# Kernel optimization log

Measured on AMD Instinct MI355X. Metric: run time of the kernel, lower is better.

The kernel has to match this reference:

```python
import jax, jax.numpy as jnp
import numpy as np

ALPHA = 2.0 / 5.0  # GRU-flow z scaling (Neural Flows, Bilos et al.)
BETA = 4.0 / 5.0   # GRU-flow r scaling


def setup_inputs() -> dict:
    key = jax.random.key(0)
    ks = jax.random.split(key, 16)
    B, T, Ds, Da, H, LF = 4096, 200, 32, 8, 128, 2

    def rn(k, shape, scale=0.1):
        return jax.random.normal(k, shape, dtype=jnp.float32) * scale

    return dict(
        s=rn(ks[0], (B, T, Ds), 1.0),
        a=rn(ks[1], (B, T, Da), 1.0),
        t=jax.random.uniform(ks[2], (B, T), dtype=jnp.float32),
        flow_Wr=rn(ks[3], (LF, H + 1, H)),
        flow_br=rn(ks[4], (LF, H)),
        flow_Wz=rn(ks[5], (LF, H + 1, H)),
        flow_bz=rn(ks[6], (LF, H)),
        flow_Wh=rn(ks[7], (LF, H + 1, H)),
        flow_bh=rn(ks[8], (LF, H)),
        flow_time_w=rn(ks[9], (LF, H), 1.0),
        gru_Wih=rn(ks[10], (3 * H, Ds + Da)),
        gru_Whh=rn(ks[11], (3 * H, H)),
        gru_bih=rn(ks[12], (3 * H,)),
        gru_bhh=rn(ks[13], (3 * H,)),
        dec_W=rn(ks[14], (Ds, H)),
        dec_b=rn(ks[15], (Ds,)),
    )


def reference(s, a, t, flow_Wr, flow_br, flow_Wz, flow_bz, flow_Wh, flow_bh,
              flow_time_w, gru_Wih, gru_Whh, gru_bih, gru_bhh, dec_W, dec_b):
    B, T, Ds = s.shape
    H = gru_Whh.shape[1]
    n_flow = flow_Wr.shape[0]

    def flow_block(h, tt, l):
        # h: [B,H], tt: [B,1]
        inp = jnp.concatenate([h, tt], axis=-1)                       # [B,H+1]
        r = BETA * jax.nn.sigmoid(inp @ flow_Wr[l] + flow_br[l])
        z = ALPHA * jax.nn.sigmoid(inp @ flow_Wz[l] + flow_bz[l])
        u = jnp.tanh(jnp.concatenate([r * h, tt], -1) @ flow_Wh[l] + flow_bh[l])
        phi = jnp.tanh(flow_time_w[l] * tt)                           # TimeTanh, phi(0)=0
        return h + phi * z * (u - h)

    def step(h, xs):
        s_i, a_i, t_i = xs                                            # [B,Ds],[B,Da],[B]
        tt = t_i[:, None]
        for l in range(n_flow):
            h = flow_block(h, tt, l)
        hid = h                                                       # stored hidden = flow output
        x = jnp.concatenate([s_i, a_i], axis=-1)                      # mode='truth'
        gi = x @ gru_Wih.T + gru_bih                                  # [B,3H]
        gh = h @ gru_Whh.T + gru_bhh
        r = jax.nn.sigmoid(gi[:, :H] + gh[:, :H])
        z = jax.nn.sigmoid(gi[:, H:2 * H] + gh[:, H:2 * H])
        n = jnp.tanh(gi[:, 2 * H:] + r * gh[:, 2 * H:])
        h_new = (1.0 - z) * n + z * h                                 # torch GRU update
        o = h_new @ dec_W.T + dec_b
        return h_new, (o, hid)

    h0 = jnp.zeros((B, H), dtype=s.dtype)
    xs = (jnp.swapaxes(s, 0, 1), jnp.swapaxes(a, 0, 1), jnp.swapaxes(t, 0, 1))
    _, (outs, hids) = jax.lax.scan(step, h0, xs)
    return jnp.swapaxes(outs, 0, 1), jnp.swapaxes(hids, 0, 1)
```

## Files before the change

### kernel.cpp

```cpp
#include <hip/hip_runtime.h>
#include <hip/hip_bf16.h>

typedef __attribute__((ext_vector_type(8))) short short8;
typedef __attribute__((ext_vector_type(4))) float f32x4;
typedef unsigned short u16;

#define NB   4096
#define TT   200
#define DS   32
#define DA   8
#define HH   128
#define HP   136
#define XP   72
#define BB   16
#define NTHR 512

#define OW_R 0
#define OW_Z 33024
#define OW_H 66048
#define OB_R 99072
#define OB_Z 99328
#define OB_H 99584
#define OTW  99840
#define OWIH 100096
#define OWHH 124672
#define OBIH 173824
#define OBHH 174208
#define ODW  174592
#define ODB  178688
#define NPK  178720
#define OFF2 16512
#define HIDOFF ((size_t)NB * TT * DS)

__device__ __forceinline__ float bf2f(u16 u){
  union { unsigned int i; float f; } v; v.i = ((unsigned int)u) << 16; return v.f;
}
__device__ __forceinline__ u16 f2bf(float f){
  __hip_bfloat16 h = __float2bfloat16(f);
  return *reinterpret_cast<u16*>(&h);
}
__device__ __forceinline__ float sigm(float x){
  return __builtin_amdgcn_rcpf(1.f + __expf(-x));
}
__device__ __forceinline__ float tanh_(float x){
  return 1.f - 2.f * __builtin_amdgcn_rcpf(1.f + __expf(2.f * x));
}
__device__ __forceinline__ float scrub(float x){
  return fminf(8.f, fmaxf(-8.f, x));
}

__global__ void detect_kernel(const void* t_in, int* ws_flag){
  int lane = threadIdx.x;
  u16 v = ((const u16*)t_in)[2 * lane];
  float f = bf2f(v);
  bool ok = (f >= 0.0009765625f) && (f < 1.0f);
  unsigned long long m = __ballot(ok);
  if (lane == 0) ws_flag[0] = (__popcll(m) < 32) ? 1 : 0;
}

__global__ void conv_kernel(const void* Wr, const void* Wz, const void* Wh,
                            const void* br, const void* bz, const void* bh,
                            const void* tw, const void* Wih, const void* Whh,
                            const void* bih, const void* bhh,
                            const void* dW, const void* db_, void* ws){
  const int flag = *(const int*)ws;
  u16* dst = (u16*)ws + 8;
  int i = blockIdx.x * 256 + threadIdx.x;
  if (i >= NPK) return;
  auto cv = [&](const void* p, int li) -> u16 {
    if (flag) return f2bf(((const float*)p)[li]);
    return ((const u16*)p)[li];
  };
  u16 v;
  if      (i < OW_Z) v = cv(Wr,  i - OW_R);
  else if (i < OW_H) v = cv(Wz,  i - OW_Z);
  else if (i < OB_R) v = cv(Wh,  i - OW_H);
  else if (i < OB_Z) v = cv(br,  i - OB_R);
  else if (i < OB_H) v = cv(bz,  i - OB_Z);
  else if (i < OTW)  v = cv(bh,  i - OB_H);
  else if (i < OWIH) v = cv(tw,  i - OTW);
  else if (i < OWHH) { int li = i - OWIH; int n = li >> 6, k = li & 63;
                       v = (k < 40) ? cv(Wih, n * 40 + k) : (u16)0; }
  else if (i < OBIH) v = cv(Whh, i - OWHH);
  else if (i < OBHH) v = cv(bih, i - OBIH);
  else if (i < ODW)  v = cv(bhh, i - OBHH);
  else if (i < ODB)  v = cv(dW,  i - ODW);
  else               v = cv(db_, i - ODB);
  dst[i] = v;
}

__global__ __launch_bounds__(NTHR, 2)
void odernn_kernel(const void* __restrict__ s_in, const void* __restrict__ a_in,
                   const void* __restrict__ t_in, void* __restrict__ out,
                   const void* __restrict__ ws){
  __shared__ alignas(16) u16 h_sh[2][BB][HP];
  __shared__ alignas(16) u16 rh_sh[BB][HP];
  __shared__ alignas(16) u16 x_sh[BB][XP];
  __shared__ float t_sh[BB];

  const int flag = *(const int*)ws;
  const u16* pk  = (const u16*)ws + 8;

  const int tid  = threadIdx.x;
  const int w    = tid >> 6;
  const int lane = tid & 63;
  const int q    = lane >> 4;
  const int m16  = lane & 15;
  const int col  = (w << 4) | m16;
  const int row4 = q << 2;
  const int b0   = blockIdx.x * BB;
  const int aoff = m16 * HP + q * 8;

  for (int i = tid; i < 2*BB*HP; i += NTHR) (&h_sh[0][0][0])[i] = 0;
  for (int i = tid; i < BB*XP;   i += NTHR) (&x_sh[0][0])[i]   = 0;
  if (tid < BB){
    size_t idx = (size_t)(b0 + tid) * TT;
    float tv; if (flag) tv = ((const float*)t_in)[idx]; else tv = bf2f(((const u16*)t_in)[idx]);
    t_sh[tid] = tv;
  }

  const u16* WrP = pk + OW_R; const u16* WzP = pk + OW_Z; const u16* WhP = pk + OW_H;
  const u16* Wsrc[6] = { WrP, WzP, WhP, WrP + OFF2, WzP + OFF2, WhP + OFF2 };
  short8 fw[6][4];
  float fwl[6], fb[6];
#pragma unroll
  for (int m = 0; m < 6; ++m){
#pragma unroll
    for (int ks = 0; ks < 4; ++ks){
      short8 v;
#pragma unroll
      for (int j = 0; j < 8; ++j)
        v[j] = (short)Wsrc[m][(ks*32 + q*8 + j)*HH + col];
      fw[m][ks] = v;
    }
    fwl[m] = bf2f(Wsrc[m][128*HH + col]);
  }
  fb[0] = bf2f(pk[OB_R + col]);      fb[1] = bf2f(pk[OB_Z + col]);      fb[2] = bf2f(pk[OB_H + col]);
  fb[3] = bf2f(pk[OB_R + HH + col]); fb[4] = bf2f(pk[OB_Z + HH + col]); fb[5] = bf2f(pk[OB_H + HH + col]);
  const float ftw0 = bf2f(pk[OTW + col]), ftw1 = bf2f(pk[OTW + HH + col]);

  short8 whhf[3][4];
#pragma unroll
  for (int g = 0; g < 3; ++g){
    const u16* base = pk + OWHH + (size_t)(g*HH + col) * HH;
#pragma unroll
    for (int ks = 0; ks < 4; ++ks)
      whhf[g][ks] = *reinterpret_cast<const short8*>(base + ks*32 + q*8);
  }
  const float bs_r = bf2f(pk[OBIH + col])      + bf2f(pk[OBHH + col]);
  const float bs_z = bf2f(pk[OBIH + HH + col]) + bf2f(pk[OBHH + HH + col]);
  const float bi_n = bf2f(pk[OBIH + 2*HH + col]);
  const float bh_n = bf2f(pk[OBHH + 2*HH + col]);
  const float db   = bf2f(pk[ODB + (col & 31)]);

  float hv[4] = {0.f, 0.f, 0.f, 0.f};
  int cur = 0;
  __syncthreads();

  for (int t = 0; t < TT; ++t){
    const u16* h_in = &h_sh[cur][0][0];
    float tt4[4];
#pragma unroll
    for (int r = 0; r < 4; ++r) tt4[r] = t_sh[row4 + r];

    if (w < 2 && t > 0){
      f32x4 oacc = {0.f,0.f,0.f,0.f};
#pragma unroll
      for (int ks = 0; ks < 4; ++ks){
        short8 da  = *reinterpret_cast<const short8*>(h_in + aoff + ks*32);
        short8 dbw = *reinterpret_cast<const short8*>(pk + ODW + col*HH + ks*32 + q*8);
        oacc = __builtin_amdgcn_mfma_f32_16x16x32_bf16(da, dbw, oacc, 0, 0, 0);
      }
#pragma unroll
      for (int r = 0; r < 4; ++r){
        size_t oidx = ((size_t)(b0 + row4 + r)*TT + (t - 1))*DS + col;
        float val = oacc[r] + db;
        if (flag) ((float*)out)[oidx] = val; else ((u16*)out)[oidx] = f2bf(val);
      }
    }

#pragma unroll
    for (int l = 0; l < 2; ++l){
      const u16* hr = &h_sh[cur][0][0];
      u16* hw = &h_sh[cur ^ 1][0][0];
      short8 ha[4];
#pragma unroll
      for (int ks = 0; ks < 4; ++ks)
        ha[ks] = *reinterpret_cast<const short8*>(hr + aoff + ks*32);
      f32x4 racc = {0.f,0.f,0.f,0.f}, zacc = {0.f,0.f,0.f,0.f};
#pragma unroll
      for (int ks = 0; ks < 4; ++ks){
        racc = __builtin_amdgcn_mfma_f32_16x16x32_bf16(ha[ks], fw[3*l+0][ks], racc, 0, 0, 0);
        zacc = __builtin_amdgcn_mfma_f32_16x16x32_bf16(ha[ks], fw[3*l+1][ks], zacc, 0, 0, 0);
      }
      float zv[4];
#pragma unroll
      for (int r = 0; r < 4; ++r){
        float rv = 0.8f * sigm(racc[r] + tt4[r]*fwl[3*l+0] + fb[3*l+0]);
        zv[r]    = 0.4f * sigm(zacc[r] + tt4[r]*fwl[3*l+1] + fb[3*l+1]);
        rh_sh[row4 + r][col] = f2bf(rv * hv[r]);
      }
      if (l == 1){
        { int row = tid >> 5, c = tid & 31;
          size_t sidx = ((size_t)(b0 + row)*TT + t)*DS + c;
          float sv; if (flag) sv = ((const float*)s_in)[sidx]; else sv = bf2f(((const u16*)s_in)[sidx]);
          x_sh[row][c] = f2bf(sv); }
        if (tid < BB*DA){ int row = tid >> 3, c = tid & 7;
          size_t aidx = ((size_t)(b0 + row)*TT + t)*DA + c;
          float av; if (flag) av = ((const float*)a_in)[aidx]; else av = bf2f(((const u16*)a_in)[aidx]);
          x_sh[row][DS + c] = f2bf(av); }
      }
      __syncthreads();
      short8 ua[4];
#pragma unroll
      for (int ks = 0; ks < 4; ++ks)
        ua[ks] = *reinterpret_cast<const short8*>(&rh_sh[0][0] + aoff + ks*32);
      f32x4 uacc = {0.f,0.f,0.f,0.f};
#pragma unroll
      for (int ks = 0; ks < 4; ++ks)
        uacc = __builtin_amdgcn_mfma_f32_16x16x32_bf16(ua[ks], fw[3*l+2][ks], uacc, 0, 0, 0);
      const float ftwl = l ? ftw1 : ftw0;
#pragma unroll
      for (int r = 0; r < 4; ++r){
        float u   = tanh_(uacc[r] + tt4[r]*fwl[3*l+2] + fb[3*l+2]);
        float phi = tanh_(ftwl * tt4[r]);
        hv[r] = scrub(hv[r] + phi * zv[r] * (u - hv[r]));
        hw[(row4 + r)*HP + col] = f2bf(hv[r]);
      }
      __syncthreads();
      cur ^= 1;
    }

    {
      const u16* hg = &h_sh[cur][0][0];
      u16* hw = &h_sh[cur ^ 1][0][0];
#pragma unroll
      for (int r = 0; r < 4; ++r){
        size_t hidx = HIDOFF + ((size_t)(b0 + row4 + r)*TT + t)*HH + col;
        if (flag) ((float*)out)[hidx] = hv[r]; else ((u16*)out)[hidx] = f2bf(hv[r]);
      }
      if (tid < BB && t + 1 < TT){
        size_t idx = (size_t)(b0 + tid)*TT + t + 1;
        float tv; if (flag) tv = ((const float*)t_in)[idx]; else tv = bf2f(((const u16*)t_in)[idx]);
        t_sh[tid] = tv;
      }

      short8 xa[2];
#pragma unroll
      for (int ks = 0; ks < 2; ++ks)
        xa[ks] = *reinterpret_cast<const short8*>(&x_sh[0][0] + m16*XP + ks*32 + q*8);
      f32x4 ar = {0.f,0.f,0.f,0.f}, az = {0.f,0.f,0.f,0.f};
      f32x4 agin = {0.f,0.f,0.f,0.f}, aghn = {0.f,0.f,0.f,0.f};
      const u16* wr_ih = pk + OWIH + (size_t)col*64;
      const u16* wz_ih = pk + OWIH + (size_t)(HH + col)*64;
      const u16* wn_ih = pk + OWIH + (size_t)(2*HH + col)*64;
#pragma unroll
      for (int ks = 0; ks < 2; ++ks){
        const int kb = ks*32 + q*8;
        ar   = __builtin_amdgcn_mfma_f32_16x16x32_bf16(xa[ks], *reinterpret_cast<const short8*>(wr_ih + kb), ar,   0,0,0);
        az   = __builtin_amdgcn_mfma_f32_16x16x32_bf16(xa[ks], *reinterpret_cast<const short8*>(wz_ih + kb), az,   0,0,0);
        agin = __builtin_amdgcn_mfma_f32_16x16x32_bf16(xa[ks], *reinterpret_cast<const short8*>(wn_ih + kb), agin, 0,0,0);
      }
      short8 hgf[4];
#pragma unroll
      for (int ks = 0; ks < 4; ++ks)
        hgf[ks] = *reinterpret_cast<const short8*>(hg + aoff + ks*32);
#pragma unroll
      for (int ks = 0; ks < 4; ++ks){
        ar   = __builtin_amdgcn_mfma_f32_16x16x32_bf16(hgf[ks], whhf[0][ks], ar,   0,0,0);
        az   = __builtin_amdgcn_mfma_f32_16x16x32_bf16(hgf[ks], whhf[1][ks], az,   0,0,0);
        aghn = __builtin_amdgcn_mfma_f32_16x16x32_bf16(hgf[ks], whhf[2][ks], aghn, 0,0,0);
      }
#pragma unroll
      for (int r = 0; r < 4; ++r){
        float gr = sigm(ar[r] + bs_r);
        float gz = sigm(az[r] + bs_z);
        float gn = tanh_(agin[r] + bi_n + gr*(aghn[r] + bh_n));
        hv[r] = scrub((1.f - gz)*gn + gz*hv[r]);
        hw[(row4 + r)*HP + col] = f2bf(hv[r]);
      }
      __syncthreads();
      cur ^= 1;
    }
  }

  if (w < 2){
    const u16* h_in = &h_sh[cur][0][0];
    f32x4 oacc = {0.f,0.f,0.f,0.f};
#pragma unroll
    for (int ks = 0; ks < 4; ++ks){
      short8 da  = *reinterpret_cast<const short8*>(h_in + aoff + ks*32);
      short8 dbw = *reinterpret_cast<const short8*>(pk + ODW + col*HH + ks*32 + q*8);
      oacc = __builtin_amdgcn_mfma_f32_16x16x32_bf16(da, dbw, oacc, 0, 0, 0);
    }
#pragma unroll
    for (int r = 0; r < 4; ++r){
      size_t oidx = ((size_t)(b0 + row4 + r)*TT + (TT - 1))*DS + col;
      float val = oacc[r] + db;
      if (flag) ((float*)out)[oidx] = val; else ((u16*)out)[oidx] = f2bf(val);
    }
  }
}

extern "C" void kernel_launch(void* const* d_in, const int* in_sizes, int n_in,
                              void* d_out, int out_size, void* d_ws, size_t ws_size,
                              hipStream_t stream){
  detect_kernel<<<1, 64, 0, stream>>>(d_in[2], (int*)d_ws);
  conv_kernel<<<(NPK + 255)/256, 256, 0, stream>>>(d_in[3], d_in[5], d_in[7],
                                                   d_in[4], d_in[6], d_in[8],
                                                   d_in[9], d_in[10], d_in[11],
                                                   d_in[12], d_in[13], d_in[14],
                                                   d_in[15], d_ws);
  odernn_kernel<<<dim3(NB/BB), dim3(NTHR), 0, stream>>>(
      d_in[0], d_in[1], d_in[2], d_out, d_ws);
}
```

Measured before the change: 1.346 ms.

## Halve batch tile, stream pre-transposed weights from global, prefetch inputs

The batch tile drops from 16 to 8 rows and the block from 512 to 256 threads, so twice as many blocks run. The flow weights are pre-transposed in the packing kernel into a column-major layout and no longer held in registers; every MFMA now loads its B operand from global/L2 and computes two 16-column tiles per wave. The s/a inputs for the next step are prefetched into registers. The aim is to cut register pressure and raise occupancy, at the cost of repeated weight loads each step and half-wasted MFMA rows, since only 8 of the 16 A rows are real.

```diff
diff --git a/kernel.cpp b/kernel.cpp
--- a/kernel.cpp
+++ b/kernel.cpp
@@ -12,24 +12,22 @@
 #define HH   128
 #define HP   136
 #define XP   72
-#define BB   16
-#define NTHR 512
-
-#define OW_R 0
-#define OW_Z 33024
-#define OW_H 66048
-#define OB_R 99072
-#define OB_Z 99328
-#define OB_H 99584
-#define OTW  99840
-#define OWIH 100096
-#define OWHH 124672
-#define OBIH 173824
-#define OBHH 174208
-#define ODW  174592
-#define ODB  178688
-#define NPK  178720
-#define OFF2 16512
+#define BB   8
+#define NTHR 256
+
+#define PFW   0
+#define PFWL  98304
+#define PFB   99072
+#define PTW   99840
+#define PWIH  100096
+#define PWHH  124672
+#define PBIH  173824
+#define PBHH  174208
+#define PDW   174592
+#define PDB   178688
+#define NPK   178720
+#define FSTRIDE 16512
+
 #define HIDOFF ((size_t)NB * TT * DS)
 
 __device__ __forceinline__ float bf2f(u16 u){
@@ -48,6 +46,10 @@
 __device__ __forceinline__ float scrub(float x){
   return fminf(8.f, fmaxf(-8.f, x));
 }
+__device__ __forceinline__ short8 ld8(const u16* p){
+  return *reinterpret_cast<const short8*>(p);
+}
+#define MFMA __builtin_amdgcn_mfma_f32_16x16x32_bf16
 
 __global__ void detect_kernel(const void* t_in, int* ws_flag){
   int lane = threadIdx.x;
@@ -71,21 +73,26 @@
     if (flag) return f2bf(((const float*)p)[li]);
     return ((const u16*)p)[li];
   };
+  const void* FG[3]  = { Wr, Wz, Wh };
+  const void* FBp[3] = { br, bz, bh };
   u16 v;
-  if      (i < OW_Z) v = cv(Wr,  i - OW_R);
-  else if (i < OW_H) v = cv(Wz,  i - OW_Z);
-  else if (i < OB_R) v = cv(Wh,  i - OW_H);
-  else if (i < OB_Z) v = cv(br,  i - OB_R);
-  else if (i < OB_H) v = cv(bz,  i - OB_Z);
-  else if (i < OTW)  v = cv(bh,  i - OB_H);
-  else if (i < OWIH) v = cv(tw,  i - OTW);
-  else if (i < OWHH) { int li = i - OWIH; int n = li >> 6, k = li & 63;
-                       v = (k < 40) ? cv(Wih, n * 40 + k) : (u16)0; }
-  else if (i < OBIH) v = cv(Whh, i - OWHH);
-  else if (i < OBHH) v = cv(bih, i - OBIH);
-  else if (i < ODW)  v = cv(bhh, i - OBHH);
-  else if (i < ODB)  v = cv(dW,  i - ODW);
-  else               v = cv(db_, i - ODB);
+  if (i < PFWL){ int m = i >> 14, r = i & 16383, col = r >> 7, k = r & 127;
+                 int l = m / 3, g = m % 3;
+                 v = cv(FG[g], l*FSTRIDE + k*HH + col); }
+  else if (i < PFB){ int li = i - PFWL; int m = li >> 7, col = li & 127;
+                 int l = m / 3, g = m % 3;
+                 v = cv(FG[g], l*FSTRIDE + HH*HH + col); }
+  else if (i < PTW){ int li = i - PFB; int m = li >> 7, col = li & 127;
+                 int l = m / 3, g = m % 3;
+                 v = cv(FBp[g], l*HH + col); }
+  else if (i < PWIH){ v = cv(tw, i - PTW); }
+  else if (i < PWHH){ int li = i - PWIH; int n = li >> 6, k = li & 63;
+                 v = (k < 40) ? cv(Wih, n*40 + k) : (u16)0; }
+  else if (i < PBIH){ v = cv(Whh, i - PWHH); }
+  else if (i < PBHH){ v = cv(bih, i - PBIH); }
+  else if (i < PDW) { v = cv(bhh, i - PBHH); }
+  else if (i < PDB) { v = cv(dW,  i - PDW); }
+  else              { v = cv(db_, i - PDB); }
   dst[i] = v;
 }
 
@@ -93,10 +100,10 @@
 void odernn_kernel(const void* __restrict__ s_in, const void* __restrict__ a_in,
                    const void* __restrict__ t_in, void* __restrict__ out,
                    const void* __restrict__ ws){
-  __shared__ alignas(16) u16 h_sh[2][BB][HP];
-  __shared__ alignas(16) u16 rh_sh[BB][HP];
-  __shared__ alignas(16) u16 x_sh[BB][XP];
-  __shared__ float t_sh[BB];
+  __shared__ alignas(16) u16 h_sh[2][8][HP];
+  __shared__ alignas(16) u16 rh_sh[8][HP];
+  __shared__ alignas(16) u16 x_sh[8][XP];
+  __shared__ float t_sh[8];
 
   const int flag = *(const int*)ws;
   const u16* pk  = (const u16*)ws + 8;
@@ -106,76 +113,82 @@
   const int lane = tid & 63;
   const int q    = lane >> 4;
   const int m16  = lane & 15;
-  const int col  = (w << 4) | m16;
-  const int row4 = q << 2;
+  const bool hi  = (q >= 2);
+  const int row4 = (q & 1) << 2;
+  const int colm = (w << 5) + ((q >> 1) << 4) + m16;
+  const int aoff  = (m16 & 7) * HP + (q << 3);
+  const int aoffx = (m16 & 7) * XP + (q << 3);
   const int b0   = blockIdx.x * BB;
-  const int aoff = m16 * HP + q * 8;
-
-  for (int i = tid; i < 2*BB*HP; i += NTHR) (&h_sh[0][0][0])[i] = 0;
-  for (int i = tid; i < BB*XP;   i += NTHR) (&x_sh[0][0])[i]   = 0;
+
+  for (int i = tid; i < 2*8*HP; i += NTHR) (&h_sh[0][0][0])[i] = 0;
+  for (int i = tid; i < 8*XP;   i += NTHR) (&x_sh[0][0])[i]   = 0;
   if (tid < BB){
     size_t idx = (size_t)(b0 + tid) * TT;
-    float tv; if (flag) tv = ((const float*)t_in)[idx]; else tv = bf2f(((const u16*)t_in)[idx]);
-    t_sh[tid] = tv;
+    t_sh[tid] = flag ? ((const float*)t_in)[idx] : bf2f(((const u16*)t_in)[idx]);
   }
 
-  const u16* WrP = pk + OW_R; const u16* WzP = pk + OW_Z; const u16* WhP = pk + OW_H;
-  const u16* Wsrc[6] = { WrP, WzP, WhP, WrP + OFF2, WzP + OFF2, WhP + OFF2 };
-  short8 fw[6][4];
   float fwl[6], fb[6];
 #pragma unroll
   for (int m = 0; m < 6; ++m){
-#pragma unroll
-    for (int ks = 0; ks < 4; ++ks){
-      short8 v;
-#pragma unroll
-      for (int j = 0; j < 8; ++j)
-        v[j] = (short)Wsrc[m][(ks*32 + q*8 + j)*HH + col];
-      fw[m][ks] = v;
-    }
-    fwl[m] = bf2f(Wsrc[m][128*HH + col]);
+    fwl[m] = bf2f(pk[PFWL + m*HH + colm]);
+    fb[m]  = bf2f(pk[PFB  + m*HH + colm]);
   }
-  fb[0] = bf2f(pk[OB_R + col]);      fb[1] = bf2f(pk[OB_Z + col]);      fb[2] = bf2f(pk[OB_H + col]);
-  fb[3] = bf2f(pk[OB_R + HH + col]); fb[4] = bf2f(pk[OB_Z + HH + col]); fb[5] = bf2f(pk[OB_H + HH + col]);
-  const float ftw0 = bf2f(pk[OTW + col]), ftw1 = bf2f(pk[OTW + HH + col]);
-
-  short8 whhf[3][4];
-#pragma unroll
-  for (int g = 0; g < 3; ++g){
-    const u16* base = pk + OWHH + (size_t)(g*HH + col) * HH;
-#pragma unroll
-    for (int ks = 0; ks < 4; ++ks)
-      whhf[g][ks] = *reinterpret_cast<const short8*>(base + ks*32 + q*8);
-  }
-  const float bs_r = bf2f(pk[OBIH + col])      + bf2f(pk[OBHH + col]);
-  const float bs_z = bf2f(pk[OBIH + HH + col]) + bf2f(pk[OBHH + HH + col]);
-  const float bi_n = bf2f(pk[OBIH + 2*HH + col]);
-  const float bh_n = bf2f(pk[OBHH + 2*HH + col]);
-  const float db   = bf2f(pk[ODB + (col & 31)]);
+  const float ftw0 = bf2f(pk[PTW + colm]);
+  const float ftw1 = bf2f(pk[PTW + HH + colm]);
+  const float bs_r = bf2f(pk[PBIH + colm])      + bf2f(pk[PBHH + colm]);
+  const float bs_z = bf2f(pk[PBIH + HH + colm]) + bf2f(pk[PBHH + HH + colm]);
+  const float bi_n = bf2f(pk[PBIH + 2*HH + colm]);
+  const float bh_n = bf2f(pk[PBHH + 2*HH + colm]);
+  const float db   = bf2f(pk[PDB + ((w & 1) << 4) + m16]);
+
+  int fB[6][2], whB[3][2], wiB[3][2];
+#pragma unroll
+  for (int m = 0; m < 6; ++m)
+#pragma unroll
+    for (int c = 0; c < 2; ++c)
+      fB[m][c] = PFW + m*16384 + (((w*2 + c)*16 + m16) << 7) + (q << 3);
+#pragma unroll
+  for (int g = 0; g < 3; ++g)
+#pragma unroll
+    for (int c = 0; c < 2; ++c){
+      whB[g][c] = PWHH + ((g*HH + (w*2 + c)*16 + m16) << 7) + (q << 3);
+      wiB[g][c] = PWIH + ((g*HH + (w*2 + c)*16 + m16) << 6) + (q << 3);
+    }
+  const int dwB = PDW + (((w & 1)*16 + m16) << 7) + (q << 3);
+
+  float sP, aP = 0.f;
+  { int row = tid >> 5, c = tid & 31;
+    size_t sidx = ((size_t)(b0 + row)*TT + 0)*DS + c;
+    sP = flag ? ((const float*)s_in)[sidx] : bf2f(((const u16*)s_in)[sidx]); }
+  if (tid < 64){ int row = tid >> 3, c = tid & 7;
+    size_t aidx = ((size_t)(b0 + row)*TT + 0)*DA + c;
+    aP = flag ? ((const float*)a_in)[aidx] : bf2f(((const u16*)a_in)[aidx]); }
 
   float hv[4] = {0.f, 0.f, 0.f, 0.f};
   int cur = 0;
   __syncthreads();
 
   for (int t = 0; t < TT; ++t){
-    const u16* h_in = &h_sh[cur][0][0];
     float tt4[4];
 #pragma unroll
     for (int r = 0; r < 4; ++r) tt4[r] = t_sh[row4 + r];
 
     if (w < 2 && t > 0){
-      f32x4 oacc = {0.f,0.f,0.f,0.f};
+      const u16* hr = &h_sh[cur][0][0];
+      f32x4 oa = {0.f,0.f,0.f,0.f};
 #pragma unroll
       for (int ks = 0; ks < 4; ++ks){
-        short8 da  = *reinterpret_cast<const short8*>(h_in + aoff + ks*32);
-        short8 dbw = *reinterpret_cast<const short8*>(pk + ODW + col*HH + ks*32 + q*8);
-        oacc = __builtin_amdgcn_mfma_f32_16x16x32_bf16(da, dbw, oacc, 0, 0, 0);
-      }
-#pragma unroll
-      for (int r = 0; r < 4; ++r){
-        size_t oidx = ((size_t)(b0 + row4 + r)*TT + (t - 1))*DS + col;
-        float val = oacc[r] + db;
-        if (flag) ((float*)out)[oidx] = val; else ((u16*)out)[oidx] = f2bf(val);
+        short8 haf = *reinterpret_cast<const short8*>(hr + aoff + ks*32);
+        short8 bw  = ld8(pk + dwB + ks*32);
+        oa = MFMA(haf, bw, oa, 0, 0, 0);
+      }
+      if (q < 2){
+#pragma unroll
+        for (int r = 0; r < 4; ++r){
+          size_t oidx = ((size_t)(b0 + (q<<2) + r)*TT + (t-1))*DS + ((w&1)<<4) + m16;
+          float val = oa[r] + db;
+          if (flag) ((float*)out)[oidx] = val; else ((u16*)out)[oidx] = f2bf(val);
+        }
       }
     }
 
@@ -187,45 +200,55 @@
 #pragma unroll
       for (int ks = 0; ks < 4; ++ks)
         ha[ks] = *reinterpret_cast<const short8*>(hr + aoff + ks*32);
-      f32x4 racc = {0.f,0.f,0.f,0.f}, zacc = {0.f,0.f,0.f,0.f};
+      f32x4 r0={0.f,0.f,0.f,0.f}, r1={0.f,0.f,0.f,0.f};
+      f32x4 z0={0.f,0.f,0.f,0.f}, z1={0.f,0.f,0.f,0.f};
 #pragma unroll
       for (int ks = 0; ks < 4; ++ks){
-        racc = __builtin_amdgcn_mfma_f32_16x16x32_bf16(ha[ks], fw[3*l+0][ks], racc, 0, 0, 0);
-        zacc = __builtin_amdgcn_mfma_f32_16x16x32_bf16(ha[ks], fw[3*l+1][ks], zacc, 0, 0, 0);
+        r0 = MFMA(ha[ks], ld8(pk + fB[3*l+0][0] + ks*32), r0, 0,0,0);
+        r1 = MFMA(ha[ks], ld8(pk + fB[3*l+0][1] + ks*32), r1, 0,0,0);
+        z0 = MFMA(ha[ks], ld8(pk + fB[3*l+1][0] + ks*32), z0, 0,0,0);
+        z1 = MFMA(ha[ks], ld8(pk + fB[3*l+1][1] + ks*32), z1, 0,0,0);
       }
       float zv[4];
 #pragma unroll
       for (int r = 0; r < 4; ++r){
-        float rv = 0.8f * sigm(racc[r] + tt4[r]*fwl[3*l+0] + fb[3*l+0]);
-        zv[r]    = 0.4f * sigm(zacc[r] + tt4[r]*fwl[3*l+1] + fb[3*l+1]);
-        rh_sh[row4 + r][col] = f2bf(rv * hv[r]);
+        float ra = hi ? r1[r] : r0[r];
+        float za = hi ? z1[r] : z0[r];
+        float rv = 0.8f * sigm(ra + tt4[r]*fwl[3*l+0] + fb[3*l+0]);
+        zv[r]    = 0.4f * sigm(za + tt4[r]*fwl[3*l+1] + fb[3*l+1]);
+        rh_sh[row4 + r][colm] = f2bf(rv * hv[r]);
       }
       if (l == 1){
-        { int row = tid >> 5, c = tid & 31;
-          size_t sidx = ((size_t)(b0 + row)*TT + t)*DS + c;
-          float sv; if (flag) sv = ((const float*)s_in)[sidx]; else sv = bf2f(((const u16*)s_in)[sidx]);
-          x_sh[row][c] = f2bf(sv); }
-        if (tid < BB*DA){ int row = tid >> 3, c = tid & 7;
-          size_t aidx = ((size_t)(b0 + row)*TT + t)*DA + c;
-          float av; if (flag) av = ((const float*)a_in)[aidx]; else av = bf2f(((const u16*)a_in)[aidx]);
-          x_sh[row][DS + c] = f2bf(av); }
+        { int row = tid >> 5, c = tid & 31; x_sh[row][c] = f2bf(sP); }
+        if (tid < 64){ int row = tid >> 3, c = tid & 7; x_sh[row][DS + c] = f2bf(aP); }
+        if (t + 1 < TT){
+          int row = tid >> 5, c = tid & 31;
+          size_t sidx = ((size_t)(b0 + row)*TT + (t+1))*DS + c;
+          sP = flag ? ((const float*)s_in)[sidx] : bf2f(((const u16*)s_in)[sidx]);
+          if (tid < 64){ int r2 = tid >> 3, c2 = tid & 7;
+            size_t aidx = ((size_t)(b0 + r2)*TT + (t+1))*DA + c2;
+            aP = flag ? ((const float*)a_in)[aidx] : bf2f(((const u16*)a_in)[aidx]); }
+        }
       }
       __syncthreads();
       short8 ua[4];
 #pragma unroll
       for (int ks = 0; ks < 4; ++ks)
         ua[ks] = *reinterpret_cast<const short8*>(&rh_sh[0][0] + aoff + ks*32);
-      f32x4 uacc = {0.f,0.f,0.f,0.f};
-#pragma unroll
-      for (int ks = 0; ks < 4; ++ks)
-        uacc = __builtin_amdgcn_mfma_f32_16x16x32_bf16(ua[ks], fw[3*l+2][ks], uacc, 0, 0, 0);
+      f32x4 u0={0.f,0.f,0.f,0.f}, u1={0.f,0.f,0.f,0.f};
+#pragma unroll
+      for (int ks = 0; ks < 4; ++ks){
+        u0 = MFMA(ua[ks], ld8(pk + fB[3*l+2][0] + ks*32), u0, 0,0,0);
+        u1 = MFMA(ua[ks], ld8(pk + fB[3*l+2][1] + ks*32), u1, 0,0,0);
+      }
       const float ftwl = l ? ftw1 : ftw0;
 #pragma unroll
       for (int r = 0; r < 4; ++r){
-        float u   = tanh_(uacc[r] + tt4[r]*fwl[3*l+2] + fb[3*l+2]);
+        float ume = hi ? u1[r] : u0[r];
+        float u   = tanh_(ume + tt4[r]*fwl[3*l+2] + fb[3*l+2]);
         float phi = tanh_(ftwl * tt4[r]);
         hv[r] = scrub(hv[r] + phi * zv[r] * (u - hv[r]));
-        hw[(row4 + r)*HP + col] = f2bf(hv[r]);
+        hw[(row4 + r)*HP + colm] = f2bf(hv[r]);
       }
       __syncthreads();
       cur ^= 1;
@@ -234,50 +257,54 @@
     {
       const u16* hg = &h_sh[cur][0][0];
       u16* hw = &h_sh[cur ^ 1][0][0];
-#pragma unroll
-      for (int r = 0; r < 4; ++r){
-        size_t hidx = HIDOFF + ((size_t)(b0 + row4 + r)*TT + t)*HH + col;
-        if (flag) ((float*)out)[hidx] = hv[r]; else ((u16*)out)[hidx] = f2bf(hv[r]);
+      short8 xa[2];
+#pragma unroll
+      for (int ks = 0; ks < 2; ++ks)
+        xa[ks] = *reinterpret_cast<const short8*>(&x_sh[0][0] + aoffx + ks*32);
+      short8 hgf[4];
+#pragma unroll
+      for (int ks = 0; ks < 4; ++ks)
+        hgf[ks] = *reinterpret_cast<const short8*>(hg + aoff + ks*32);
+      f32x4 ar0={0.f,0.f,0.f,0.f}, ar1={0.f,0.f,0.f,0.f};
+      f32x4 az0={0.f,0.f,0.f,0.f}, az1={0.f,0.f,0.f,0.f};
+      f32x4 an0={0.f,0.f,0.f,0.f}, an1={0.f,0.f,0.f,0.f};
+      f32x4 ah0={0.f,0.f,0.f,0.f}, ah1={0.f,0.f,0.f,0.f};
+#pragma unroll
+      for (int ks = 0; ks < 2; ++ks){
+        ar0 = MFMA(xa[ks], ld8(pk + wiB[0][0] + ks*32), ar0, 0,0,0);
+        ar1 = MFMA(xa[ks], ld8(pk + wiB[0][1] + ks*32), ar1, 0,0,0);
+        az0 = MFMA(xa[ks], ld8(pk + wiB[1][0] + ks*32), az0, 0,0,0);
+        az1 = MFMA(xa[ks], ld8(pk + wiB[1][1] + ks*32), az1, 0,0,0);
+        an0 = MFMA(xa[ks], ld8(pk + wiB[2][0] + ks*32), an0, 0,0,0);
+        an1 = MFMA(xa[ks], ld8(pk + wiB[2][1] + ks*32), an1, 0,0,0);
+      }
+#pragma unroll
+      for (int ks = 0; ks < 4; ++ks){
+        ar0 = MFMA(hgf[ks], ld8(pk + whB[0][0] + ks*32), ar0, 0,0,0);
+        ar1 = MFMA(hgf[ks], ld8(pk + whB[0][1] + ks*32), ar1, 0,0,0);
+        az0 = MFMA(hgf[ks], ld8(pk + whB[1][0] + ks*32), az0, 0,0,0);
+        az1 = MFMA(hgf[ks], ld8(pk + whB[1][1] + ks*32), az1, 0,0,0);
+        ah0 = MFMA(hgf[ks], ld8(pk + whB[2][0] + ks*32), ah0, 0,0,0);
+        ah1 = MFMA(hgf[ks], ld8(pk + whB[2][1] + ks*32), ah1, 0,0,0);
       }
       if (tid < BB && t + 1 < TT){
         size_t idx = (size_t)(b0 + tid)*TT + t + 1;
-        float tv; if (flag) tv = ((const float*)t_in)[idx]; else tv = bf2f(((const u16*)t_in)[idx]);
-        t_sh[tid] = tv;
-      }
-
-      short8 xa[2];
-#pragma unroll
-      for (int ks = 0; ks < 2; ++ks)
-        xa[ks] = *reinterpret_cast<const short8*>(&x_sh[0][0] + m16*XP + ks*32 + q*8);
-      f32x4 ar = {0.f,0.f,0.f,0.f}, az = {0.f,0.f,0.f,0.f};
-      f32x4 agin = {0.f,0.f,0.f,0.f}, aghn = {0.f,0.f,0.f,0.f};
-      const u16* wr_ih = pk + OWIH + (size_t)col*64;
-      const u16* wz_ih = pk + OWIH + (size_t)(HH + col)*64;
-      const u16* wn_ih = pk + OWIH + (size_t)(2*HH + col)*64;
-#pragma unroll
-      for (int ks = 0; ks < 2; ++ks){
-        const int kb = ks*32 + q*8;
-        ar   = __builtin_amdgcn_mfma_f32_16x16x32_bf16(xa[ks], *reinterpret_cast<const short8*>(wr_ih + kb), ar,   0,0,0);
-        az   = __builtin_amdgcn_mfma_f32_16x16x32_bf16(xa[ks], *reinterpret_cast<const short8*>(wz_ih + kb), az,   0,0,0);
-        agin = __builtin_amdgcn_mfma_f32_16x16x32_bf16(xa[ks], *reinterpret_cast<const short8*>(wn_ih + kb), agin, 0,0,0);
-      }
-      short8 hgf[4];
-#pragma unroll
-      for (int ks = 0; ks < 4; ++ks)
-        hgf[ks] = *reinterpret_cast<const short8*>(hg + aoff + ks*32);
-#pragma unroll
-      for (int ks = 0; ks < 4; ++ks){
-        ar   = __builtin_amdgcn_mfma_f32_16x16x32_bf16(hgf[ks], whhf[0][ks], ar,   0,0,0);
-        az   = __builtin_amdgcn_mfma_f32_16x16x32_bf16(hgf[ks], whhf[1][ks], az,   0,0,0);
-        aghn = __builtin_amdgcn_mfma_f32_16x16x32_bf16(hgf[ks], whhf[2][ks], aghn, 0,0,0);
+        t_sh[tid] = flag ? ((const float*)t_in)[idx] : bf2f(((const u16*)t_in)[idx]);
       }
 #pragma unroll
       for (int r = 0; r < 4; ++r){
-        float gr = sigm(ar[r] + bs_r);
-        float gz = sigm(az[r] + bs_z);
-        float gn = tanh_(agin[r] + bi_n + gr*(aghn[r] + bh_n));
-        hv[r] = scrub((1.f - gz)*gn + gz*hv[r]);
-        hw[(row4 + r)*HP + col] = f2bf(hv[r]);
+        float arm = hi ? ar1[r] : ar0[r];
+        float azm = hi ? az1[r] : az0[r];
+        float anm = hi ? an1[r] : an0[r];
+        float ahm = hi ? ah1[r] : ah0[r];
+        float hpre = hv[r];
+        size_t hidx = HIDOFF + ((size_t)(b0 + row4 + r)*TT + t)*HH + colm;
+        if (flag) ((float*)out)[hidx] = hpre; else ((u16*)out)[hidx] = f2bf(hpre);
+        float gr = sigm(arm + bs_r);
+        float gz = sigm(azm + bs_z);
+        float gn = tanh_(anm + bi_n + gr*(ahm + bh_n));
+        hv[r] = scrub((1.f - gz)*gn + gz*hpre);
+        hw[(row4 + r)*HP + colm] = f2bf(hv[r]);
       }
       __syncthreads();
       cur ^= 1;
@@ -285,19 +312,21 @@
   }
 
   if (w < 2){
-    const u16* h_in = &h_sh[cur][0][0];
-    f32x4 oacc = {0.f,0.f,0.f,0.f};
+    const u16* hr = &h_sh[cur][0][0];
+    f32x4 oa = {0.f,0.f,0.f,0.f};
 #pragma unroll
     for (int ks = 0; ks < 4; ++ks){
-      short8 da  = *reinterpret_cast<const short8*>(h_in + aoff + ks*32);
-      short8 dbw = *reinterpret_cast<const short8*>(pk + ODW + col*HH + ks*32 + q*8);
-      oacc = __builtin_amdgcn_mfma_f32_16x16x32_bf16(da, dbw, oacc, 0, 0, 0);
-    }
-#pragma unroll
-    for (int r = 0; r < 4; ++r){
-      size_t oidx = ((size_t)(b0 + row4 + r)*TT + (TT - 1))*DS + col;
-      float val = oacc[r] + db;
-      if (flag) ((float*)out)[oidx] = val; else ((u16*)out)[oidx] = f2bf(val);
+      short8 haf = *reinterpret_cast<const short8*>(hr + aoff + ks*32);
+      short8 bw  = ld8(pk + dwB + ks*32);
+      oa = MFMA(haf, bw, oa, 0, 0, 0);
+    }
+    if (q < 2){
+#pragma unroll
+      for (int r = 0; r < 4; ++r){
+        size_t oidx = ((size_t)(b0 + (q<<2) + r)*TT + (TT-1))*DS + ((w&1)<<4) + m16;
+        float val = oa[r] + db;
+        if (flag) ((float*)out)[oidx] = val; else ((u16*)out)[oidx] = f2bf(val);
+      }
     }
   }
 }
```

Result: slower. 4.075 ms (+202.8%).

## Split batch tile into two 8-row groups with duplicated A rows per MFMA

Applied to the files above, without the earlier changes.

Reorganizes the 16-row batch tile into two groups of 8 rows, each loaded with rows duplicated across the 16-row MFMA A operand so each lane keeps only 2 useful outputs per group. This doubles MFMA count per step, apparently to interleave two independent chains and shorten dependency latency. It also prefetches the next step's s/a inputs into registers a step ahead, reloads Wih weights from global each step instead of keeping them inline, and spreads decoder output over four waves. The risk is doubled matrix work and extra register pressure for little gain in a latency-bound recurrence.

```diff
diff --git a/kernel.cpp b/kernel.cpp
--- a/kernel.cpp
+++ b/kernel.cpp
@@ -13,6 +13,7 @@
 #define HP   136
 #define XP   72
 #define BB   16
+#define GS   8
 #define NTHR 512
 
 #define OW_R 0
@@ -48,6 +49,10 @@
 __device__ __forceinline__ float scrub(float x){
   return fminf(8.f, fmaxf(-8.f, x));
 }
+__device__ __forceinline__ short8 ld8(const u16* p){
+  return *reinterpret_cast<const short8*>(p);
+}
+#define MFMA __builtin_amdgcn_mfma_f32_16x16x32_bf16
 
 __global__ void detect_kernel(const void* t_in, int* ws_flag){
   int lane = threadIdx.x;
@@ -93,9 +98,9 @@
 void odernn_kernel(const void* __restrict__ s_in, const void* __restrict__ a_in,
                    const void* __restrict__ t_in, void* __restrict__ out,
                    const void* __restrict__ ws){
-  __shared__ alignas(16) u16 h_sh[2][BB][HP];
-  __shared__ alignas(16) u16 rh_sh[BB][HP];
-  __shared__ alignas(16) u16 x_sh[BB][XP];
+  __shared__ alignas(16) u16 h_sh[2][2][GS][HP];
+  __shared__ alignas(16) u16 rh_sh[2][GS][HP];
+  __shared__ alignas(16) u16 x_sh[2][GS][XP];
   __shared__ float t_sh[BB];
 
   const int flag = *(const int*)ws;
@@ -107,16 +112,17 @@
   const int q    = lane >> 4;
   const int m16  = lane & 15;
   const int col  = (w << 4) | m16;
-  const int row4 = q << 2;
+  const bool hiq = (q >= 2);
+  const int rowL = ((q & 1) << 2) | ((q >> 1) << 1);
+  const int aoff  = (m16 & 7) * HP + (q << 3);
+  const int aoffx = (m16 & 7) * XP + (q << 3);
   const int b0   = blockIdx.x * BB;
-  const int aoff = m16 * HP + q * 8;
-
-  for (int i = tid; i < 2*BB*HP; i += NTHR) (&h_sh[0][0][0])[i] = 0;
-  for (int i = tid; i < BB*XP;   i += NTHR) (&x_sh[0][0])[i]   = 0;
+
+  for (int i = tid; i < 2*2*GS*HP; i += NTHR) (&h_sh[0][0][0][0])[i] = 0;
+  for (int i = tid; i < 2*GS*XP;   i += NTHR) (&x_sh[0][0][0])[i]   = 0;
   if (tid < BB){
     size_t idx = (size_t)(b0 + tid) * TT;
-    float tv; if (flag) tv = ((const float*)t_in)[idx]; else tv = bf2f(((const u16*)t_in)[idx]);
-    t_sh[tid] = tv;
+    t_sh[tid] = flag ? ((const float*)t_in)[idx] : bf2f(((const u16*)t_in)[idx]);
   }
 
   const u16* WrP = pk + OW_R; const u16* WzP = pk + OW_Z; const u16* WhP = pk + OW_H;
@@ -153,150 +159,188 @@
   const float bh_n = bf2f(pk[OBHH + 2*HH + col]);
   const float db   = bf2f(pk[ODB + (col & 31)]);
 
-  float hv[4] = {0.f, 0.f, 0.f, 0.f};
+  float sP, aP = 0.f;
+  { int row = tid >> 5, c = tid & 31;
+    size_t sidx = (size_t)(b0 + row)*TT*DS + c;
+    sP = flag ? ((const float*)s_in)[sidx] : bf2f(((const u16*)s_in)[sidx]); }
+  if (tid < BB*DA){ int row = tid >> 3, c = tid & 7;
+    size_t aidx = (size_t)(b0 + row)*TT*DA + c;
+    aP = flag ? ((const float*)a_in)[aidx] : bf2f(((const u16*)a_in)[aidx]); }
+
+  float hv[2][2] = {{0.f,0.f},{0.f,0.f}};
   int cur = 0;
   __syncthreads();
 
   for (int t = 0; t < TT; ++t){
-    const u16* h_in = &h_sh[cur][0][0];
-    float tt4[4];
-#pragma unroll
-    for (int r = 0; r < 4; ++r) tt4[r] = t_sh[row4 + r];
-
-    if (w < 2 && t > 0){
-      f32x4 oacc = {0.f,0.f,0.f,0.f};
+    float tt[2][2];
+#pragma unroll
+    for (int g = 0; g < 2; ++g)
+#pragma unroll
+      for (int r = 0; r < 2; ++r) tt[g][r] = t_sh[g*GS + rowL + r];
+
+    if (w < 4 && t > 0){
+      const u16* hr = &h_sh[cur][w >> 1][0][0];
+      f32x4 oa = {0.f,0.f,0.f,0.f};
 #pragma unroll
       for (int ks = 0; ks < 4; ++ks){
-        short8 da  = *reinterpret_cast<const short8*>(h_in + aoff + ks*32);
-        short8 dbw = *reinterpret_cast<const short8*>(pk + ODW + col*HH + ks*32 + q*8);
-        oacc = __builtin_amdgcn_mfma_f32_16x16x32_bf16(da, dbw, oacc, 0, 0, 0);
+        short8 haf = ld8(hr + aoff + ks*32);
+        short8 bw  = ld8(pk + ODW + (col & 31)*HH + ks*32 + q*8);
+        oa = MFMA(haf, bw, oa, 0, 0, 0);
       }
 #pragma unroll
-      for (int r = 0; r < 4; ++r){
-        size_t oidx = ((size_t)(b0 + row4 + r)*TT + (t - 1))*DS + col;
-        float val = oacc[r] + db;
+      for (int r = 0; r < 2; ++r){
+        float val = (hiq ? oa[2+r] : oa[r]) + db;
+        size_t oidx = ((size_t)(b0 + (w>>1)*GS + rowL + r)*TT + (t-1))*DS + (col & 31);
         if (flag) ((float*)out)[oidx] = val; else ((u16*)out)[oidx] = f2bf(val);
       }
     }
 
 #pragma unroll
     for (int l = 0; l < 2; ++l){
-      const u16* hr = &h_sh[cur][0][0];
-      u16* hw = &h_sh[cur ^ 1][0][0];
-      short8 ha[4];
-#pragma unroll
-      for (int ks = 0; ks < 4; ++ks)
-        ha[ks] = *reinterpret_cast<const short8*>(hr + aoff + ks*32);
-      f32x4 racc = {0.f,0.f,0.f,0.f}, zacc = {0.f,0.f,0.f,0.f};
-#pragma unroll
-      for (int ks = 0; ks < 4; ++ks){
-        racc = __builtin_amdgcn_mfma_f32_16x16x32_bf16(ha[ks], fw[3*l+0][ks], racc, 0, 0, 0);
-        zacc = __builtin_amdgcn_mfma_f32_16x16x32_bf16(ha[ks], fw[3*l+1][ks], zacc, 0, 0, 0);
-      }
-      float zv[4];
-#pragma unroll
-      for (int r = 0; r < 4; ++r){
-        float rv = 0.8f * sigm(racc[r] + tt4[r]*fwl[3*l+0] + fb[3*l+0]);
-        zv[r]    = 0.4f * sigm(zacc[r] + tt4[r]*fwl[3*l+1] + fb[3*l+1]);
-        rh_sh[row4 + r][col] = f2bf(rv * hv[r]);
-      }
+      short8 ha[2][4];
+#pragma unroll
+      for (int g = 0; g < 2; ++g)
+#pragma unroll
+        for (int ks = 0; ks < 4; ++ks)
+          ha[g][ks] = ld8(&h_sh[cur][g][0][0] + aoff + ks*32);
+      f32x4 rA[2] = {{0.f,0.f,0.f,0.f},{0.f,0.f,0.f,0.f}};
+      f32x4 zA[2] = {{0.f,0.f,0.f,0.f},{0.f,0.f,0.f,0.f}};
+#pragma unroll
+      for (int g = 0; g < 2; ++g)
+#pragma unroll
+        for (int ks = 0; ks < 4; ++ks){
+          rA[g] = MFMA(ha[g][ks], fw[3*l+0][ks], rA[g], 0,0,0);
+          zA[g] = MFMA(ha[g][ks], fw[3*l+1][ks], zA[g], 0,0,0);
+        }
+      float zv[2][2];
+#pragma unroll
+      for (int g = 0; g < 2; ++g)
+#pragma unroll
+        for (int r = 0; r < 2; ++r){
+          float rm = hiq ? rA[g][2+r] : rA[g][r];
+          float zm = hiq ? zA[g][2+r] : zA[g][r];
+          float rv = 0.8f * sigm(rm + tt[g][r]*fwl[3*l+0] + fb[3*l+0]);
+          zv[g][r] = 0.4f * sigm(zm + tt[g][r]*fwl[3*l+1] + fb[3*l+1]);
+          rh_sh[g][rowL + r][col] = f2bf(rv * hv[g][r]);
+        }
       if (l == 1){
-        { int row = tid >> 5, c = tid & 31;
-          size_t sidx = ((size_t)(b0 + row)*TT + t)*DS + c;
-          float sv; if (flag) sv = ((const float*)s_in)[sidx]; else sv = bf2f(((const u16*)s_in)[sidx]);
-          x_sh[row][c] = f2bf(sv); }
-        if (tid < BB*DA){ int row = tid >> 3, c = tid & 7;
-          size_t aidx = ((size_t)(b0 + row)*TT + t)*DA + c;
-          float av; if (flag) av = ((const float*)a_in)[aidx]; else av = bf2f(((const u16*)a_in)[aidx]);
-          x_sh[row][DS + c] = f2bf(av); }
+        { int row = tid >> 5, c = tid & 31; x_sh[row>>3][row&7][c] = f2bf(sP); }
+        if (tid < BB*DA){ int row = tid >> 3, c = tid & 7; x_sh[row>>3][row&7][DS + c] = f2bf(aP); }
+        if (t + 1 < TT){
+          int row = tid >> 5, c = tid & 31;
+          size_t sidx = ((size_t)(b0 + row)*TT + (t+1))*DS + c;
+          sP = flag ? ((const float*)s_in)[sidx] : bf2f(((const u16*)s_in)[sidx]);
+          if (tid < BB*DA){ int r2 = tid >> 3, c2 = tid & 7;
+            size_t aidx = ((size_t)(b0 + r2)*TT + (t+1))*DA + c2;
+            aP = flag ? ((const float*)a_in)[aidx] : bf2f(((const u16*)a_in)[aidx]); }
+        }
       }
       __syncthreads();
-      short8 ua[4];
-#pragma unroll
-      for (int ks = 0; ks < 4; ++ks)
-        ua[ks] = *reinterpret_cast<const short8*>(&rh_sh[0][0] + aoff + ks*32);
-      f32x4 uacc = {0.f,0.f,0.f,0.f};
-#pragma unroll
-      for (int ks = 0; ks < 4; ++ks)
-        uacc = __builtin_amdgcn_mfma_f32_16x16x32_bf16(ua[ks], fw[3*l+2][ks], uacc, 0, 0, 0);
+      short8 ua[2][4];
+#pragma unroll
+      for (int g = 0; g < 2; ++g)
+#pragma unroll
+        for (int ks = 0; ks < 4; ++ks)
+          ua[g][ks] = ld8(&rh_sh[g][0][0] + aoff + ks*32);
+      f32x4 uA[2] = {{0.f,0.f,0.f,0.f},{0.f,0.f,0.f,0.f}};
+#pragma unroll
+      for (int g = 0; g < 2; ++g)
+#pragma unroll
+        for (int ks = 0; ks < 4; ++ks)
+          uA[g] = MFMA(ua[g][ks], fw[3*l+2][ks], uA[g], 0,0,0);
       const float ftwl = l ? ftw1 : ftw0;
 #pragma unroll
-      for (int r = 0; r < 4; ++r){
-        float u   = tanh_(uacc[r] + tt4[r]*fwl[3*l+2] + fb[3*l+2]);
-        float phi = tanh_(ftwl * tt4[r]);
-        hv[r] = scrub(hv[r] + phi * zv[r] * (u - hv[r]));
-        hw[(row4 + r)*HP + col] = f2bf(hv[r]);
-      }
+      for (int g = 0; g < 2; ++g)
+#pragma unroll
+        for (int r = 0; r < 2; ++r){
+          float um  = hiq ? uA[g][2+r] : uA[g][r];
+          float u   = tanh_(um + tt[g][r]*fwl[3*l+2] + fb[3*l+2]);
+          float phi = tanh_(ftwl * tt[g][r]);
+          hv[g][r] = scrub(hv[g][r] + phi * zv[g][r] * (u - hv[g][r]));
+          h_sh[cur ^ 1][g][rowL + r][col] = f2bf(hv[g][r]);
+        }
       __syncthreads();
       cur ^= 1;
     }
 
     {
-      const u16* hg = &h_sh[cur][0][0];
-      u16* hw = &h_sh[cur ^ 1][0][0];
-#pragma unroll
-      for (int r = 0; r < 4; ++r){
-        size_t hidx = HIDOFF + ((size_t)(b0 + row4 + r)*TT + t)*HH + col;
-        if (flag) ((float*)out)[hidx] = hv[r]; else ((u16*)out)[hidx] = f2bf(hv[r]);
-      }
+      short8 wihf[3][2];
+#pragma unroll
+      for (int gg = 0; gg < 3; ++gg)
+#pragma unroll
+        for (int ks = 0; ks < 2; ++ks)
+          wihf[gg][ks] = ld8(pk + OWIH + (size_t)(gg*HH + col)*64 + ks*32 + q*8);
+      short8 xa[2][2];
+#pragma unroll
+      for (int g = 0; g < 2; ++g)
+#pragma unroll
+        for (int ks = 0; ks < 2; ++ks)
+          xa[g][ks] = ld8(&x_sh[g][0][0] + aoffx + ks*32);
+      short8 hgf[2][4];
+#pragma unroll
+      for (int g = 0; g < 2; ++g)
+#pragma unroll
+        for (int ks = 0; ks < 4; ++ks)
+          hgf[g][ks] = ld8(&h_sh[cur][g][0][0] + aoff + ks*32);
+      f32x4 ar[2] = {{0.f,0.f,0.f,0.f},{0.f,0.f,0.f,0.f}};
+      f32x4 az[2] = {{0.f,0.f,0.f,0.f},{0.f,0.f,0.f,0.f}};
+      f32x4 an[2] = {{0.f,0.f,0.f,0.f},{0.f,0.f,0.f,0.f}};
+      f32x4 ah[2] = {{0.f,0.f,0.f,0.f},{0.f,0.f,0.f,0.f}};
+#pragma unroll
+      for (int g = 0; g < 2; ++g)
+#pragma unroll
+        for (int ks = 0; ks < 2; ++ks){
+          ar[g] = MFMA(xa[g][ks], wihf[0][ks], ar[g], 0,0,0);
+          az[g] = MFMA(xa[g][ks], wihf[1][ks], az[g], 0,0,0);
+          an[g] = MFMA(xa[g][ks], wihf[2][ks], an[g], 0,0,0);
+        }
+#pragma unroll
+      for (int g = 0; g < 2; ++g)
+#pragma unroll
+        for (int ks = 0; ks < 4; ++ks){
+          ar[g] = MFMA(hgf[g][ks], whhf[0][ks], ar[g], 0,0,0);
+          az[g] = MFMA(hgf[g][ks], whhf[1][ks], az[g], 0,0,0);
+          ah[g] = MFMA(hgf[g][ks], whhf[2][ks], ah[g], 0,0,0);
+        }
       if (tid < BB && t + 1 < TT){
         size_t idx = (size_t)(b0 + tid)*TT + t + 1;
-        float tv; if (flag) tv = ((const float*)t_in)[idx]; else tv = bf2f(((const u16*)t_in)[idx]);
-        t_sh[tid] = tv;
+        t_sh[tid] = flag ? ((const float*)t_in)[idx] : bf2f(((const u16*)t_in)[idx]);
       }
-
-      short8 xa[2];
-#pragma unroll
-      for (int ks = 0; ks < 2; ++ks)
-        xa[ks] = *reinterpret_cast<const short8*>(&x_sh[0][0] + m16*XP + ks*32 + q*8);
-      f32x4 ar = {0.f,0.f,0.f,0.f}, az = {0.f,0.f,0.f,0.f};
-      f32x4 agin = {0.f,0.f,0.f,0.f}, aghn = {0.f,0.f,0.f,0.f};
-      const u16* wr_ih = pk + OWIH + (size_t)col*64;
-      const u16* wz_ih = pk + OWIH + (size_t)(HH + col)*64;
-      const u16* wn_ih = pk + OWIH + (size_t)(2*HH + col)*64;
-#pragma unroll
-      for (int ks = 0; ks < 2; ++ks){
-        const int kb = ks*32 + q*8;
-        ar   = __builtin_amdgcn_mfma_f32_16x16x32_bf16(xa[ks], *reinterpret_cast<const short8*>(wr_ih + kb), ar,   0,0,0);
-        az   = __builtin_amdgcn_mfma_f32_16x16x32_bf16(xa[ks], *reinterpret_cast<const short8*>(wz_ih + kb), az,   0,0,0);
-        agin = __builtin_amdgcn_mfma_f32_16x16x32_bf16(xa[ks], *reinterpret_cast<const short8*>(wn_ih + kb), agin, 0,0,0);
-      }
-      short8 hgf[4];
-#pragma unroll
-      for (int ks = 0; ks < 4; ++ks)
-        hgf[ks] = *reinterpret_cast<const short8*>(hg + aoff + ks*32);
-#pragma unroll
-      for (int ks = 0; ks < 4; ++ks){
-        ar   = __builtin_amdgcn_mfma_f32_16x16x32_bf16(hgf[ks], whhf[0][ks], ar,   0,0,0);
-        az   = __builtin_amdgcn_mfma_f32_16x16x32_bf16(hgf[ks], whhf[1][ks], az,   0,0,0);
-        aghn = __builtin_amdgcn_mfma_f32_16x16x32_bf16(hgf[ks], whhf[2][ks], aghn, 0,0,0);
-      }
-#pragma unroll
-      for (int r = 0; r < 4; ++r){
-        float gr = sigm(ar[r] + bs_r);
-        float gz = sigm(az[r] + bs_z);
-        float gn = tanh_(agin[r] + bi_n + gr*(aghn[r] + bh_n));
-        hv[r] = scrub((1.f - gz)*gn + gz*hv[r]);
-        hw[(row4 + r)*HP + col] = f2bf(hv[r]);
-      }
+#pragma unroll
+      for (int g = 0; g < 2; ++g)
+#pragma unroll
+        for (int r = 0; r < 2; ++r){
+          float arm = hiq ? ar[g][2+r] : ar[g][r];
+          float azm = hiq ? az[g][2+r] : az[g][r];
+          float anm = hiq ? an[g][2+r] : an[g][r];
+          float ahm = hiq ? ah[g][2+r] : ah[g][r];
+          float hpre = hv[g][r];
+          size_t hidx = HIDOFF + ((size_t)(b0 + g*GS + rowL + r)*TT + t)*HH + col;
+          if (flag) ((float*)out)[hidx] = hpre; else ((u16*)out)[hidx] = f2bf(hpre);
+          float gr = sigm(arm + bs_r);
+          float gz = sigm(azm + bs_z);
+          float gn = tanh_(anm + bi_n + gr*(ahm + bh_n));
+          hv[g][r] = scrub((1.f - gz)*gn + gz*hpre);
+          h_sh[cur ^ 1][g][rowL + r][col] = f2bf(hv[g][r]);
+        }
       __syncthreads();
       cur ^= 1;
     }
   }
 
-  if (w < 2){
-    const u16* h_in = &h_sh[cur][0][0];
-    f32x4 oacc = {0.f,0.f,0.f,0.f};
+  if (w < 4){
+    const u16* hr = &h_sh[cur][w >> 1][0][0];
+    f32x4 oa = {0.f,0.f,0.f,0.f};
 #pragma unroll
     for (int ks = 0; ks < 4; ++ks){
-      short8 da  = *reinterpret_cast<const short8*>(h_in + aoff + ks*32);
-      short8 dbw = *reinterpret_cast<const short8*>(pk + ODW + col*HH + ks*32 + q*8);
-      oacc = __builtin_amdgcn_mfma_f32_16x16x32_bf16(da, dbw, oacc, 0, 0, 0);
-    }
-#pragma unroll
-    for (int r = 0; r < 4; ++r){
-      size_t oidx = ((size_t)(b0 + row4 + r)*TT + (TT - 1))*DS + col;
-      float val = oacc[r] + db;
+      short8 haf = ld8(hr + aoff + ks*32);
+      short8 bw  = ld8(pk + ODW + (col & 31)*HH + ks*32 + q*8);
+      oa = MFMA(haf, bw, oa, 0, 0, 0);
+    }
+#pragma unroll
+    for (int r = 0; r < 2; ++r){
+      float val = (hiq ? oa[2+r] : oa[r]) + db;
+      size_t oidx = ((size_t)(b0 + (w>>1)*GS + rowL + r)*TT + (TT-1))*DS + (col & 31);
       if (flag) ((float*)out)[oidx] = val; else ((u16*)out)[oidx] = f2bf(val);
     }
   }
```

Result: slower. 2.412 ms (+79.2%).
